# Performance work log

Measured on AMD Instinct MI355X. Metric: run time of the kernel, lower is better.

The kernel has to match this reference:

```python
import jax, jax.numpy as jnp
import numpy as np

N = 100_000      # nodes
E = 1_600_000    # graph edges
M = 10_000       # hyperedges
I = 800_000      # hypergraph incidences
F_IN = 128
HID = 128


def _lin(key, fan_in, fan_out):
    return (jax.random.normal(key, (fan_in, fan_out), jnp.float32) / np.sqrt(fan_in)).astype(jnp.float32)


def setup_inputs() -> dict:
    key = jax.random.key(0)
    ks = jax.random.split(key, 14)
    x = jax.random.normal(ks[0], (N, F_IN), jnp.float32)
    edge_index = jax.random.randint(ks[1], (2, E), 0, N, dtype=jnp.int32)
    edge_weights = jax.random.uniform(ks[2], (E,), jnp.float32)
    node_idx = jax.random.randint(ks[3], (I,), 0, N, dtype=jnp.int32)
    he_idx = jax.random.randint(ks[4], (I,), 0, M, dtype=jnp.int32)
    hyperedge_index = jnp.stack([node_idx, he_idx])
    hyperedge_distances = jax.random.uniform(ks[5], (M,), jnp.float32)
    return {
        "x": x,
        "edge_index": edge_index,
        "edge_weights": edge_weights,
        "hyperedge_index": hyperedge_index,
        "hyperedge_distances": hyperedge_distances,
        "W_g1": _lin(ks[6], F_IN, HID), "b_g1": jnp.zeros((HID,), jnp.float32),
        "W_g2": _lin(ks[7], HID, HID), "b_g2": jnp.zeros((HID,), jnp.float32),
        "W_h1": _lin(ks[8], F_IN, HID), "b_h1": jnp.zeros((HID,), jnp.float32),
        "W_h2": _lin(ks[9], HID, HID), "b_h2": jnp.zeros((HID,), jnp.float32),
        "W_fc": _lin(ks[10], 2 * HID, HID), "b_fc": jnp.zeros((HID,), jnp.float32),
        "W_out": _lin(ks[11], HID, 2), "b_out": jnp.zeros((2,), jnp.float32),
    }


def _gcn(h_in, W, b, row, col, ew):
    # PyG GCNConv: lin -> sym-normalized scatter-add (self-loops included in row/col/ew) -> +bias
    h = h_in @ W
    deg = jax.ops.segment_sum(ew, col, num_segments=N)
    dis = jnp.where(deg > 0, jax.lax.rsqrt(deg), 0.0)
    norm = dis[row] * ew * dis[col]
    out = jax.ops.segment_sum(norm[:, None] * h[row], col, num_segments=N)
    return out + b


def _hyper(h_in, W, b, node_idx, he_idx):
    # PyG HypergraphConv (use_attention=False, hyperedge_weight=1):
    # out = D^{-1} H B^{-1} H^T (X W) + b
    h = h_in @ W
    D = jax.ops.segment_sum(jnp.ones((node_idx.shape[0],), h.dtype), node_idx, num_segments=N)
    Dinv = jnp.where(D > 0, 1.0 / D, 0.0)
    Bc = jax.ops.segment_sum(jnp.ones((he_idx.shape[0],), h.dtype), he_idx, num_segments=M)
    Binv = jnp.where(Bc > 0, 1.0 / Bc, 0.0)
    edge_feat = Binv[:, None] * jax.ops.segment_sum(h[node_idx], he_idx, num_segments=M)
    out = Dinv[:, None] * jax.ops.segment_sum(edge_feat[he_idx], node_idx, num_segments=N)
    return out + b


def reference(x, edge_index, edge_weights, hyperedge_index, hyperedge_distances,
              W_g1, b_g1, W_g2, b_g2, W_h1, b_h1, W_h2, b_h2,
              W_fc, b_fc, W_out, b_out):
    # add self-loops (GCNConv default add_self_loops=True, fill=1)
    loops = jnp.arange(N, dtype=edge_index.dtype)
    row = jnp.concatenate([edge_index[0], loops])
    col = jnp.concatenate([edge_index[1], loops])
    ew = jnp.concatenate([edge_weights, jnp.ones((N,), edge_weights.dtype)])

    # GCN branch (dropout = identity in eval)
    x1 = jax.nn.relu(_gcn(x, W_g1, b_g1, row, col, ew))
    x1 = jax.nn.relu(_gcn(x1, W_g2, b_g2, row, col, ew))

    # vectorized form of the per-incidence python loop:
    # node_hyperedge_weights[v] = sum over incidences (v, e) of hyperedge_distances[e]
    node_idx, he_idx = hyperedge_index[0], hyperedge_index[1]
    nhw = jax.ops.segment_sum(hyperedge_distances[he_idx], node_idx, num_segments=N)
    x2 = x * nhw[:, None]

    x2 = jax.nn.relu(_hyper(x2, W_h1, b_h1, node_idx, he_idx))
    x2 = jax.nn.relu(_hyper(x2, W_h2, b_h2, node_idx, he_idx))

    h = jnp.concatenate([x1, x2], axis=1)
    h = jax.nn.relu(h @ W_fc + b_fc)
    return h @ W_out + b_out
```

## Files before the change

kernel.cpp:

```cpp
#include <hip/hip_runtime.h>
#include <hip/hip_fp16.h>


#define THREADS 256
#define CAP_E  64
#define CAP_IN 40
#define CAP_IH 144

#define BC_E 4608
#define BC_I 2432
#define BC_H 3072

#define P1_ITEMS 16
#define P1_BLOCK 4096

typedef _Float16 half8 __attribute__((ext_vector_type(8)));
typedef float floatx4 __attribute__((ext_vector_type(4)));

#define FIX_SCALE 16777216.0f

template <int MODE>
__device__ __forceinline__ void phase1_core(
    int blk, const int* __restrict__ keys, const int* __restrict__ vals,
    const float* __restrict__ wts,
    unsigned long long* __restrict__ buf64, unsigned int* __restrict__ buf32,
    int* __restrict__ bincnt, int nitems, int nbins, int bincap,
    unsigned int* hist, unsigned int* off, unsigned int* gb, unsigned int* wsum,
    unsigned long long* reord, unsigned short* rbin) {
  const int tid = threadIdx.x;
  const int base = blk * P1_BLOCK;
  for (int i = tid; i < 512; i += 256) hist[i] = 0;
  __syncthreads();
  unsigned long long pl[P1_ITEMS];
  int bn[P1_ITEMS], lr[P1_ITEMS];
#pragma unroll
  for (int j = 0; j < P1_ITEMS; ++j) {
    int idx = base + j * 256 + tid;
    bn[j] = -1;
    if (idx < nitems) {
      int k = keys[idx], v = vals[idx];
      if (MODE == 0) {
        bn[j] = k >> 8;
        pl[j] = ((unsigned long long)__float_as_uint(wts[idx]) << 32) |
                ((unsigned long long)((unsigned int)v << 8)) |
                (unsigned long long)(k & 255);
      } else if (MODE == 1) {
        bn[j] = k >> 8;
        pl[j] = (unsigned long long)(((unsigned int)v << 8) | (unsigned int)(k & 255));
      } else {
        bn[j] = k >> 5;
        pl[j] = (unsigned long long)(((unsigned int)v << 5) | (unsigned int)(k & 31));
      }
      lr[j] = (int)atomicAdd(&hist[bn[j]], 1u);
    }
  }
  __syncthreads();
  unsigned int v0 = hist[2 * tid], v1 = hist[2 * tid + 1];
  unsigned int tsum = v0 + v1;
  unsigned int incl = tsum;
  for (int o = 1; o < 64; o <<= 1) {
    unsigned int t = __shfl_up(incl, o, 64);
    if ((tid & 63) >= o) incl += t;
  }
  if ((tid & 63) == 63) wsum[tid >> 6] = incl;
  __syncthreads();
  unsigned int woff = 0;
  for (int w = 0; w < (tid >> 6); ++w) woff += wsum[w];
  unsigned int texcl = incl - tsum + woff;
  off[2 * tid] = texcl;
  off[2 * tid + 1] = texcl + v0;
  if (2 * tid < nbins && v0) gb[2 * tid] = (unsigned int)atomicAdd(&bincnt[2 * tid], (int)v0);
  if (2 * tid + 1 < nbins && v1) gb[2 * tid + 1] = (unsigned int)atomicAdd(&bincnt[2 * tid + 1], (int)v1);
  __syncthreads();
#pragma unroll
  for (int j = 0; j < P1_ITEMS; ++j) {
    if (bn[j] >= 0) {
      unsigned int pos = off[bn[j]] + (unsigned int)lr[j];
      reord[pos] = pl[j];
      rbin[pos] = (unsigned short)bn[j];
    }
  }
  __syncthreads();
  int total = nitems - base;
  if (total > P1_BLOCK) total = P1_BLOCK;
#pragma unroll
  for (int j = 0; j < P1_ITEMS; ++j) {
    int p = j * 256 + tid;
    if (p < total) {
      int b = rbin[p];
      unsigned int idx = gb[b] + (unsigned int)p - off[b];
      if (idx < (unsigned int)bincap) {
        if (MODE == 0) buf64[(size_t)b * bincap + idx] = reord[p];
        else buf32[(size_t)b * bincap + idx] = (unsigned int)reord[p];
      }
    }
  }
}

__global__ __launch_bounds__(256) void bin_phase1_all(
    const int* __restrict__ col, const int* __restrict__ row, const float* __restrict__ ew,
    const int* __restrict__ vidx, const int* __restrict__ heidx,
    unsigned long long* __restrict__ buf_e, unsigned int* __restrict__ buf_in,
    unsigned int* __restrict__ buf_ih,
    int* __restrict__ bincnt_e, int* __restrict__ bincnt_in, int* __restrict__ bincnt_ih,
    int E, int I, int GB_E, int GB_I, int NB_E, int NB_I, int NB_H) {
  __shared__ unsigned int hist[512];
  __shared__ unsigned int off[512];
  __shared__ unsigned int gb[512];
  __shared__ unsigned int wsum[4];
  __shared__ unsigned long long reord[P1_BLOCK];
  __shared__ unsigned short rbin[P1_BLOCK];
  int b = blockIdx.x;
  if (b < GB_E)
    phase1_core<0>(b, col, row, ew, buf_e, nullptr, bincnt_e, E, NB_E, BC_E,
                   hist, off, gb, wsum, reord, rbin);
  else if (b < GB_E + GB_I)
    phase1_core<1>(b - GB_E, vidx, heidx, nullptr, nullptr, buf_in, bincnt_in, I, NB_I, BC_I,
                   hist, off, gb, wsum, reord, rbin);
  else
    phase1_core<2>(b - GB_E - GB_I, heidx, vidx, nullptr, nullptr, buf_ih, bincnt_ih, I, NB_H, BC_H,
                   hist, off, gb, wsum, reord, rbin);
}

__global__ __launch_bounds__(256) void bin_phase2_all(
    const unsigned long long* __restrict__ buf_e, const unsigned int* __restrict__ buf_in,
    const unsigned int* __restrict__ buf_ih,
    const int* __restrict__ bincnt_e, const int* __restrict__ bincnt_in,
    const int* __restrict__ bincnt_ih, const float* __restrict__ hd,
    int2* __restrict__ epairs, int* __restrict__ he_by_node, int* __restrict__ v_by_he,
    int* __restrict__ ecnt, float* __restrict__ dis,
    int* __restrict__ ncnt, float* __restrict__ nhwf, float* __restrict__ Dinv,
    int* __restrict__ hecnt, float* __restrict__ Binv,
    int N, int M, int NB_E, int NB_I) {
  __shared__ unsigned int cnt[256];
  __shared__ unsigned int aux[256];
  const int tid = threadIdx.x;
  int b = blockIdx.x;
  if (b < NB_E) {
    cnt[tid] = 0; aux[tid] = 0;
    __syncthreads();
    int tot = bincnt_e[b]; if (tot > BC_E) tot = BC_E;
    const unsigned long long* seg = buf_e + (size_t)b * BC_E;
    for (int i = tid; i < tot; i += 256) {
      unsigned long long pl = seg[i];
      int c_lo = (int)(pl & 255u);
      int r = (int)((pl >> 8) & 0xFFFFFFu);
      float w = __uint_as_float((unsigned int)(pl >> 32));
      unsigned int s = atomicAdd(&cnt[c_lo], 1u);
      atomicAdd(&aux[c_lo], (unsigned int)(w * FIX_SCALE + 0.5f));
      if (s < CAP_E)
        epairs[((size_t)b * 256 + c_lo) * CAP_E + s] = make_int2(r, __float_as_int(w));
    }
    __syncthreads();
    int v = b * 256 + tid;
    if (v < N) {
      unsigned int c = cnt[tid];
      ecnt[v] = (c < CAP_E) ? (int)c : CAP_E;
      dis[v] = rsqrtf(1.0f + (float)aux[tid] * (1.0f / FIX_SCALE));
    }
  } else if (b < NB_E + NB_I) {
    b -= NB_E;
    cnt[tid] = 0; aux[tid] = 0;
    __syncthreads();
    int tot = bincnt_in[b]; if (tot > BC_I) tot = BC_I;
    const unsigned int* seg = buf_in + (size_t)b * BC_I;
    for (int i = tid; i < tot; i += 256) {
      unsigned int pl = seg[i];
      int v_lo = (int)(pl & 255u);
      int e = (int)(pl >> 8);
      unsigned int s = atomicAdd(&cnt[v_lo], 1u);
      atomicAdd(&aux[v_lo], (unsigned int)(hd[e] * FIX_SCALE + 0.5f));
      if (s < CAP_IN) he_by_node[((size_t)b * 256 + v_lo) * CAP_IN + s] = e;
    }
    __syncthreads();
    int v = b * 256 + tid;
    if (v < N) {
      unsigned int c = cnt[tid];
      ncnt[v] = (c < CAP_IN) ? (int)c : CAP_IN;
      nhwf[v] = (float)aux[tid] * (1.0f / FIX_SCALE);
      Dinv[v] = (c > 0) ? 1.0f / (float)c : 0.0f;
    }
  } else {
    b -= NB_E + NB_I;
    if (tid < 32) cnt[tid] = 0;
    __syncthreads();
    int tot = bincnt_ih[b]; if (tot > BC_H) tot = BC_H;
    const unsigned int* seg = buf_ih + (size_t)b * BC_H;
    for (int i = tid; i < tot; i += 256) {
      unsigned int pl = seg[i];
      int e_lo = (int)(pl & 31u);
      int v = (int)(pl >> 5);
      unsigned int s = atomicAdd(&cnt[e_lo], 1u);
      if (s < CAP_IH) v_by_he[((size_t)b * 32 + e_lo) * CAP_IH + s] = v;
    }
    __syncthreads();
    if (tid < 32) {
      int e = b * 32 + tid;
      if (e < M) {
        unsigned int c = cnt[tid];
        hecnt[e] = (c < CAP_IH) ? (int)c : CAP_IH;
        Binv[e] = (c > 0) ? 1.0f / (float)c : 0.0f;
      }
    }
  }
}

__global__ void wprep_all(const float* __restrict__ Wg1, const float* __restrict__ Wg2,
                          const float* __restrict__ Wh1, const float* __restrict__ Wh2,
                          const float* __restrict__ Wfc,
                          _Float16* __restrict__ Wtg1, _Float16* __restrict__ Wtg2,
                          _Float16* __restrict__ Wth1, _Float16* __restrict__ Wth2,
                          _Float16* __restrict__ Wtfc) {
  int idx = blockIdx.x * THREADS + threadIdx.x;
  if (idx < 65536) {
    int s = idx >> 14, local = idx & 16383;
    const float* W = (s == 0) ? Wg1 : (s == 1) ? Wg2 : (s == 2) ? Wh1 : Wh2;
    _Float16* Wt = (s == 0) ? Wtg1 : (s == 1) ? Wtg2 : (s == 2) ? Wth1 : Wth2;
    int n = local >> 7, kk = local & 127;
    int k = kk ^ ((n & 7) << 3);
    Wt[local] = (_Float16)W[k * 128 + n];
  } else if (idx < 98304) {
    int local = idx - 65536;
    int n = local >> 8, kk = local & 255;
    int k = kk ^ ((n & 7) << 3);
    Wtfc[local] = (_Float16)Wfc[k * 128 + n];
  }
}

__global__ __launch_bounds__(256) void mm_dual(
    const float* __restrict__ X, const _Float16* __restrict__ Wt1,
    const _Float16* __restrict__ Wt2, const float* __restrict__ dis,
    _Float16* __restrict__ C1, _Float16* __restrict__ C2, int nrows) {
  __shared__ _Float16 WtL[2][128 * 128];
  __shared__ _Float16 ebuf[4][16 * 136];
  const int tid = threadIdx.x;
  {
    const float4* s1 = (const float4*)Wt1;
    const float4* s2 = (const float4*)Wt2;
    float4* d1 = (float4*)WtL[0];
    float4* d2 = (float4*)WtL[1];
#pragma unroll
    for (int i = 0; i < 8; ++i) { d1[tid + 256 * i] = s1[tid + 256 * i]; d2[tid + 256 * i] = s2[tid + 256 * i]; }
  }
  __syncthreads();
  const int w = tid >> 6, l = tid & 63;
  const int m = l & 15, quad = l >> 4;
  const int rbase = blockIdx.x * 256 + w * 64;
  half8 a[4][4];
#pragma unroll
  for (int r = 0; r < 4; ++r) {
    int gr = rbase + r * 16 + m;
#pragma unroll
    for (int s = 0; s < 4; ++s) {
      int ks = s * 32 + quad * 8;
      if (gr < nrows) {
        float4 f0 = *(const float4*)(X + (size_t)gr * 128 + ks);
        float4 f1 = *(const float4*)(X + (size_t)gr * 128 + ks + 4);
        half8 h;
        h[0] = (_Float16)f0.x; h[1] = (_Float16)f0.y; h[2] = (_Float16)f0.z; h[3] = (_Float16)f0.w;
        h[4] = (_Float16)f1.x; h[5] = (_Float16)f1.y; h[6] = (_Float16)f1.z; h[7] = (_Float16)f1.w;
        a[r][s] = h;
      } else {
#pragma unroll
        for (int j = 0; j < 8; ++j) a[r][s][j] = (_Float16)0.0f;
      }
    }
  }
  _Float16* eb = ebuf[w];
#pragma unroll
  for (int pass = 0; pass < 2; ++pass) {
    floatx4 acc[4][8];
#pragma unroll
    for (int r = 0; r < 4; ++r)
#pragma unroll
      for (int c = 0; c < 8; ++c)
#pragma unroll
        for (int j = 0; j < 4; ++j) acc[r][c][j] = 0.0f;
#pragma unroll
    for (int s = 0; s < 4; ++s) {
      const int ks = s * 32 + quad * 8;
#pragma unroll
      for (int c = 0; c < 8; ++c) {
        int n = c * 16 + m;
        half8 b = *(const half8*)&WtL[pass][n * 128 + (ks ^ ((n & 7) << 3))];
#pragma unroll
        for (int r = 0; r < 4; ++r)
          acc[r][c] = __builtin_amdgcn_mfma_f32_16x16x32_f16(a[r][s], b, acc[r][c], 0, 0, 0);
      }
    }
    _Float16* Cout = pass ? C2 : C1;
#pragma unroll
    for (int r = 0; r < 4; ++r) {
      float dv[4];
#pragma unroll
      for (int j = 0; j < 4; ++j) {
        int grow = rbase + r * 16 + quad * 4 + j;
        dv[j] = (pass == 0 && grow < nrows) ? dis[grow] : 1.0f;
      }
#pragma unroll
      for (int c = 0; c < 8; ++c)
#pragma unroll
        for (int j = 0; j < 4; ++j)
          eb[(quad * 4 + j) * 136 + c * 16 + m] = (_Float16)(acc[r][c][j] * dv[j]);
#pragma unroll
      for (int t = 0; t < 4; ++t) {
        int chunk = t * 64 + l;
        int rr = chunk >> 4;
        int off = (chunk & 15) * 8;
        int gr = rbase + r * 16 + rr;
        half8 v = *(const half8*)&eb[rr * 136 + off];
        if (gr < nrows) *(half8*)(Cout + (size_t)gr * 128 + off) = v;
      }
    }
  }
}

template <int SCALE>
__global__ __launch_bounds__(256) void mm_mfma(
    const _Float16* __restrict__ A, const _Float16* __restrict__ Wt,
    const float* __restrict__ scale, _Float16* __restrict__ Cout, int nrows) {
  __shared__ _Float16 WtL[128 * 128];
  __shared__ _Float16 ebuf[4][16 * 136];
  const int tid = threadIdx.x;
  {
    const float4* src = (const float4*)Wt;
    float4* dst = (float4*)WtL;
#pragma unroll
    for (int i = 0; i < 8; ++i) dst[tid + 256 * i] = src[tid + 256 * i];
  }
  __syncthreads();
  const int w = tid >> 6, l = tid & 63;
  const int m = l & 15, quad = l >> 4;
  const int rbase = blockIdx.x * 256 + w * 64;
  floatx4 acc[4][8];
#pragma unroll
  for (int r = 0; r < 4; ++r)
#pragma unroll
    for (int c = 0; c < 8; ++c)
#pragma unroll
      for (int j = 0; j < 4; ++j) acc[r][c][j] = 0.0f;
#pragma unroll
  for (int s = 0; s < 4; ++s) {
    const int ks = s * 32 + quad * 8;
    half8 a[4];
#pragma unroll
    for (int r = 0; r < 4; ++r) {
      int gr = rbase + r * 16 + m;
      if (gr < nrows) {
        a[r] = *(const half8*)(A + (size_t)gr * 128 + ks);
      } else {
#pragma unroll
        for (int j = 0; j < 8; ++j) a[r][j] = (_Float16)0.0f;
      }
    }
#pragma unroll
    for (int c = 0; c < 8; ++c) {
      int n = c * 16 + m;
      half8 b = *(const half8*)&WtL[n * 128 + (ks ^ ((n & 7) << 3))];
#pragma unroll
      for (int r = 0; r < 4; ++r)
        acc[r][c] = __builtin_amdgcn_mfma_f32_16x16x32_f16(a[r], b, acc[r][c], 0, 0, 0);
    }
  }
  _Float16* eb = ebuf[w];
#pragma unroll
  for (int r = 0; r < 4; ++r) {
    float dv[4];
#pragma unroll
    for (int j = 0; j < 4; ++j) {
      int grow = rbase + r * 16 + quad * 4 + j;
      dv[j] = (SCALE && grow < nrows) ? scale[grow] : 1.0f;
    }
#pragma unroll
    for (int c = 0; c < 8; ++c)
#pragma unroll
      for (int j = 0; j < 4; ++j)
        eb[(quad * 4 + j) * 136 + c * 16 + m] = (_Float16)(SCALE ? acc[r][c][j] * dv[j] : acc[r][c][j]);
#pragma unroll
    for (int t = 0; t < 4; ++t) {
      int chunk = t * 64 + l;
      int rr = chunk >> 4;
      int off = (chunk & 15) * 8;
      int gr = rbase + r * 16 + rr;
      half8 v = *(const half8*)&eb[rr * 136 + off];
      if (gr < nrows) *(half8*)(Cout + (size_t)gr * 128 + off) = v;
    }
  }
}

__global__ __launch_bounds__(256) void fc_head(
    const _Float16* __restrict__ A1, const _Float16* __restrict__ A2,
    const _Float16* __restrict__ Wt, const float* __restrict__ bfc,
    const float* __restrict__ Wout, const float* __restrict__ bout,
    float* __restrict__ out, int nrows) {
  __shared__ _Float16 WtL[128 * 256];
  __shared__ float WoutL[256];
  const int tid = threadIdx.x;
  {
    const float4* src = (const float4*)Wt;
    float4* dst = (float4*)WtL;
#pragma unroll
    for (int i = 0; i < 16; ++i) dst[tid + 256 * i] = src[tid + 256 * i];
    WoutL[tid] = Wout[tid];
  }
  __syncthreads();
  const int w = tid >> 6, l = tid & 63;
  const int m = l & 15, quad = l >> 4;
  const int rbase = blockIdx.x * 256 + w * 64;
  floatx4 acc[4][8];
#pragma unroll
  for (int r = 0; r < 4; ++r)
#pragma unroll
    for (int c = 0; c < 8; ++c)
#pragma unroll
      for (int j = 0; j < 4; ++j) acc[r][c][j] = 0.0f;
#pragma unroll
  for (int s = 0; s < 8; ++s) {
    const _Float16* Asrc = (s >= 4) ? A2 : A1;
    const int kl = (s >= 4) ? (s - 4) * 32 + quad * 8 : s * 32 + quad * 8;
    const int ks = s * 32 + quad * 8;
    half8 a[4];
#pragma unroll
    for (int r = 0; r < 4; ++r) {
      int gr = rbase + r * 16 + m;
      if (gr < nrows) {
        a[r] = *(const half8*)(Asrc + (size_t)gr * 128 + kl);
      } else {
#pragma unroll
        for (int j = 0; j < 8; ++j) a[r][j] = (_Float16)0.0f;
      }
    }
#pragma unroll
    for (int c = 0; c < 8; ++c) {
      int n = c * 16 + m;
      half8 b = *(const half8*)&WtL[n * 256 + (ks ^ ((n & 7) << 3))];
#pragma unroll
      for (int r = 0; r < 4; ++r)
        acc[r][c] = __builtin_amdgcn_mfma_f32_16x16x32_f16(a[r], b, acc[r][c], 0, 0, 0);
    }
  }
  float b0 = bout[0], b1 = bout[1];
  float bias_c[8];
#pragma unroll
  for (int c = 0; c < 8; ++c) bias_c[c] = bfc[c * 16 + m];
#pragma unroll
  for (int r = 0; r < 4; ++r) {
#pragma unroll
    for (int j = 0; j < 4; ++j) {
      float s0 = 0.f, s1 = 0.f;
#pragma unroll
      for (int c = 0; c < 8; ++c) {
        float h = fmaxf(acc[r][c][j] + bias_c[c], 0.f);
        int k = c * 16 + m;
        s0 = fmaf(h, WoutL[k * 2 + 0], s0);
        s1 = fmaf(h, WoutL[k * 2 + 1], s1);
      }
#pragma unroll
      for (int off = 1; off < 16; off <<= 1) {
        s0 += __shfl_xor(s0, off, 64);
        s1 += __shfl_xor(s1, off, 64);
      }
      if (m == 0) {
        int gr = rbase + r * 16 + quad * 4 + j;
        if (gr < nrows) {
          float2 o = make_float2(s0 + b0, s1 + b1);
          *(float2*)(out + (size_t)gr * 2) = o;
        }
      }
    }
  }
}

__global__ __launch_bounds__(256) void gcn_gather16(
    const _Float16* __restrict__ h, const int* __restrict__ ecnt,
    const int2* __restrict__ epairs, const float* __restrict__ dis,
    const float* __restrict__ bias, _Float16* __restrict__ out, int N) {
  int g = threadIdx.x >> 4, l = threadIdx.x & 15;
  int c = blockIdx.x * 16 + g;
  if (c >= N) return;
  const float4* h4 = (const float4*)h;
  float4 self = h4[(size_t)c * 16 + l];
  const _Float16* sp = (const _Float16*)&self;
  float acc[8];
#pragma unroll
  for (int j = 0; j < 8; ++j) acc[j] = (float)sp[j];
  int cnt = ecnt[c];
  const int2* seg = epairs + (size_t)c * CAP_E;
  int p = 0;
  for (; p + 2 <= cnt; p += 2) {
    int2 pr0 = seg[p];
    int2 pr1 = seg[p + 1];
    float4 hv0 = h4[(size_t)pr0.x * 16 + l];
    float4 hv1 = h4[(size_t)pr1.x * 16 + l];
    float w0 = __int_as_float(pr0.y), w1 = __int_as_float(pr1.y);
    const _Float16* hp0 = (const _Float16*)&hv0;
    const _Float16* hp1 = (const _Float16*)&hv1;
#pragma unroll
    for (int j = 0; j < 8; ++j) acc[j] = fmaf(w0, (float)hp0[j], acc[j]);
#pragma unroll
    for (int j = 0; j < 8; ++j) acc[j] = fmaf(w1, (float)hp1[j], acc[j]);
  }
  if (p < cnt) {
    int2 pr = seg[p];
    float wgt = __int_as_float(pr.y);
    float4 hv = h4[(size_t)pr.x * 16 + l];
    const _Float16* hp = (const _Float16*)&hv;
#pragma unroll
    for (int j = 0; j < 8; ++j) acc[j] = fmaf(wgt, (float)hp[j], acc[j]);
  }
  float dc = dis[c];
  float4 b0 = ((const float4*)bias)[2 * l];
  float4 b1 = ((const float4*)bias)[2 * l + 1];
  float bb[8] = {b0.x, b0.y, b0.z, b0.w, b1.x, b1.y, b1.z, b1.w};
  half8 ov;
#pragma unroll
  for (int j = 0; j < 8; ++j) ov[j] = (_Float16)fmaxf(fmaf(acc[j], dc, bb[j]), 0.f);
  *(half8*)(out + (size_t)c * 128 + l * 8) = ov;
}

template <int SCALED>
__global__ __launch_bounds__(256) void hyper_ef16(
    const _Float16* __restrict__ h, const int* __restrict__ hecnt,
    const int* __restrict__ v_by_he, const float* __restrict__ Binv,
    const float* __restrict__ nhwf, _Float16* __restrict__ ef, int M) {
  int g = threadIdx.x >> 4, l = threadIdx.x & 15;
  int e = blockIdx.x * 16 + g;
  if (e >= M) return;
  const float4* h4 = (const float4*)h;
  float acc[8];
#pragma unroll
  for (int j = 0; j < 8; ++j) acc[j] = 0.f;
  int cnt = hecnt[e];
  const int* seg = v_by_he + (size_t)e * CAP_IH;
  int p = 0;
  for (; p + 4 <= cnt; p += 4) {
    int v0 = seg[p], v1 = seg[p + 1], v2 = seg[p + 2], v3 = seg[p + 3];
    float4 a0 = h4[(size_t)v0 * 16 + l];
    float4 a1 = h4[(size_t)v1 * 16 + l];
    float4 a2 = h4[(size_t)v2 * 16 + l];
    float4 a3 = h4[(size_t)v3 * 16 + l];
    float s0 = 1.f, s1 = 1.f, s2 = 1.f, s3 = 1.f;
    if (SCALED) { s0 = nhwf[v0]; s1 = nhwf[v1]; s2 = nhwf[v2]; s3 = nhwf[v3]; }
    const _Float16* p0 = (const _Float16*)&a0;
    const _Float16* p1 = (const _Float16*)&a1;
    const _Float16* p2 = (const _Float16*)&a2;
    const _Float16* p3 = (const _Float16*)&a3;
    if (SCALED) {
#pragma unroll
      for (int j = 0; j < 8; ++j)
        acc[j] += s0 * (float)p0[j] + s1 * (float)p1[j] + s2 * (float)p2[j] + s3 * (float)p3[j];
    } else {
#pragma unroll
      for (int j = 0; j < 8; ++j)
        acc[j] += ((float)p0[j] + (float)p1[j]) + ((float)p2[j] + (float)p3[j]);
    }
  }
  for (; p < cnt; ++p) {
    int v = seg[p];
    float4 hv = h4[(size_t)v * 16 + l];
    const _Float16* hp = (const _Float16*)&hv;
    if (SCALED) {
      float s = nhwf[v];
#pragma unroll
      for (int j = 0; j < 8; ++j) acc[j] = fmaf(s, (float)hp[j], acc[j]);
    } else {
#pragma unroll
      for (int j = 0; j < 8; ++j) acc[j] += (float)hp[j];
    }
  }
  float bi = Binv[e];
  half8 ov;
#pragma unroll
  for (int j = 0; j < 8; ++j) ov[j] = (_Float16)(acc[j] * bi);
  *(half8*)(ef + (size_t)e * 128 + l * 8) = ov;
}

__global__ __launch_bounds__(256) void hyper_out16(
    const _Float16* __restrict__ ef, const int* __restrict__ ncnt,
    const int* __restrict__ he_by_node, const float* __restrict__ Dinv,
    const float* __restrict__ bias, _Float16* __restrict__ out, int N) {
  int g = threadIdx.x >> 4, l = threadIdx.x & 15;
  int v = blockIdx.x * 16 + g;
  if (v >= N) return;
  const float4* ef4 = (const float4*)ef;
  float acc[8];
#pragma unroll
  for (int j = 0; j < 8; ++j) acc[j] = 0.f;
  int cnt = ncnt[v];
  const int* seg = he_by_node + (size_t)v * CAP_IN;
  int p = 0;
  for (; p + 2 <= cnt; p += 2) {
    int e0 = seg[p], e1 = seg[p + 1];
    float4 a0 = ef4[(size_t)e0 * 16 + l];
    float4 a1 = ef4[(size_t)e1 * 16 + l];
    const _Float16* p0 = (const _Float16*)&a0;
    const _Float16* p1 = (const _Float16*)&a1;
#pragma unroll
    for (int j = 0; j < 8; ++j) acc[j] += (float)p0[j] + (float)p1[j];
  }
  if (p < cnt) {
    int e = seg[p];
    float4 hv = ef4[(size_t)e * 16 + l];
    const _Float16* hp = (const _Float16*)&hv;
#pragma unroll
    for (int j = 0; j < 8; ++j) acc[j] += (float)hp[j];
  }
  float di = Dinv[v];
  float4 b0 = ((const float4*)bias)[2 * l];
  float4 b1 = ((const float4*)bias)[2 * l + 1];
  float bb[8] = {b0.x, b0.y, b0.z, b0.w, b1.x, b1.y, b1.z, b1.w};
  half8 ov;
#pragma unroll
  for (int j = 0; j < 8; ++j) ov[j] = (_Float16)fmaxf(fmaf(acc[j], di, bb[j]), 0.f);
  *(half8*)(out + (size_t)v * 128 + l * 8) = ov;
}

extern "C" void kernel_launch(void* const* d_in, const int* in_sizes, int n_in,
                              void* d_out, int out_size, void* d_ws, size_t ws_size,
                              hipStream_t stream) {
  const float* x    = (const float*)d_in[0];
  const int*   eidx = (const int*)d_in[1];
  const float* ew   = (const float*)d_in[2];
  const int*   hidx = (const int*)d_in[3];
  const float* hd   = (const float*)d_in[4];
  const float* Wg1  = (const float*)d_in[5];
  const float* bg1  = (const float*)d_in[6];
  const float* Wg2  = (const float*)d_in[7];
  const float* bg2  = (const float*)d_in[8];
  const float* Wh1  = (const float*)d_in[9];
  const float* bh1  = (const float*)d_in[10];
  const float* Wh2  = (const float*)d_in[11];
  const float* bh2  = (const float*)d_in[12];
  const float* Wfc  = (const float*)d_in[13];
  const float* bfc  = (const float*)d_in[14];
  const float* Wout = (const float*)d_in[15];
  const float* bout = (const float*)d_in[16];

  const int N = in_sizes[0] / 128;
  const int E = in_sizes[2];
  const int I = in_sizes[3] / 2;
  const int M = in_sizes[4];
  const int* row   = eidx;
  const int* col   = eidx + E;
  const int* vidx  = hidx;
  const int* heidx = hidx + I;

  const int NB_E = (N + 255) >> 8;
  const int NB_I = (N + 255) >> 8;
  const int NB_H = (M + 31) >> 5;
  const int GB_E = (E + P1_BLOCK - 1) / P1_BLOCK;
  const int GB_I = (I + P1_BLOCK - 1) / P1_BLOCK;

  char* p = (char*)d_ws;
  auto alloc = [&](size_t bytes) -> void* {
    void* r = (void*)p;
    p += (bytes + 255) & ~(size_t)255;
    return r;
  };
  float* dis   = (float*)alloc((size_t)N * 4);
  float* nhwf  = (float*)alloc((size_t)N * 4);
  float* Dinv  = (float*)alloc((size_t)N * 4);
  float* Binv  = (float*)alloc((size_t)M * 4);
  int* ecnt    = (int*)alloc((size_t)N * 4);
  int* ncnt    = (int*)alloc((size_t)N * 4);
  int* hecnt   = (int*)alloc((size_t)M * 4);
  int* bincnt_e  = (int*)alloc((size_t)(NB_E + NB_I + NB_H) * 4);
  int* bincnt_in = bincnt_e + NB_E;
  int* bincnt_ih = bincnt_in + NB_I;
  int2* epairs = (int2*)alloc((size_t)N * CAP_E * 8);
  int* he_by_node = (int*)alloc((size_t)N * CAP_IN * 4);
  int* v_by_he    = (int*)alloc((size_t)M * CAP_IH * 4);
  _Float16* Bg   = (_Float16*)alloc((size_t)N * 128 * 2);
  _Float16* Bh   = (_Float16*)alloc((size_t)N * 128 * 2);
  _Float16* Btmp = (_Float16*)alloc((size_t)N * 128 * 2);
  _Float16* Bt1  = (_Float16*)alloc((size_t)N * 128 * 2);
  _Float16* Bt2  = (_Float16*)alloc((size_t)N * 128 * 2);
  _Float16* ef16 = (_Float16*)alloc((size_t)M * 128 * 2);
  _Float16* Wtg1 = (_Float16*)alloc(128 * 128 * 2);
  _Float16* Wtg2 = (_Float16*)alloc(128 * 128 * 2);
  _Float16* Wth1 = (_Float16*)alloc(128 * 128 * 2);
  _Float16* Wth2 = (_Float16*)alloc(128 * 128 * 2);
  _Float16* Wtfc = (_Float16*)alloc(128 * 256 * 2);

  unsigned long long* buf_e  = (unsigned long long*)Bt1;
  unsigned int*       buf_in = (unsigned int*)Bt2;
  unsigned int*       buf_ih = (unsigned int*)((char*)Bt2 + (4 << 20));

  wprep_all<<<384, THREADS, 0, stream>>>(Wg1, Wg2, Wh1, Wh2, Wfc, Wtg1, Wtg2, Wth1, Wth2, Wtfc);

  hipMemsetAsync(bincnt_e, 0, (size_t)(NB_E + NB_I + NB_H) * 4, stream);
  bin_phase1_all<<<GB_E + 2 * GB_I, THREADS, 0, stream>>>(
      col, row, ew, vidx, heidx, buf_e, buf_in, buf_ih,
      bincnt_e, bincnt_in, bincnt_ih, E, I, GB_E, GB_I, NB_E, NB_I, NB_H);
  bin_phase2_all<<<NB_E + NB_I + NB_H, THREADS, 0, stream>>>(
      buf_e, buf_in, buf_ih, bincnt_e, bincnt_in, bincnt_ih, hd,
      epairs, he_by_node, v_by_he, ecnt, dis, ncnt, nhwf, Dinv, hecnt, Binv,
      N, M, NB_E, NB_I);

  const int GMM = (N + 255) / 256;
  const int GN16 = (N + 15) / 16;
  const int GM16 = (M + 15) / 16;

  mm_dual<<<GMM, THREADS, 0, stream>>>(x, Wtg1, Wth1, dis, Bg, Bh, N);

  gcn_gather16<<<GN16, THREADS, 0, stream>>>(Bg, ecnt, epairs, dis, bg1, Bt1, N);
  mm_mfma<1><<<GMM, THREADS, 0, stream>>>(Bt1, Wtg2, dis, Btmp, N);
  gcn_gather16<<<GN16, THREADS, 0, stream>>>(Btmp, ecnt, epairs, dis, bg2, Bt1, N);

  hyper_ef16<1><<<GM16, THREADS, 0, stream>>>(Bh, hecnt, v_by_he, Binv, nhwf, ef16, M);
  hyper_out16<<<GN16, THREADS, 0, stream>>>(ef16, ncnt, he_by_node, Dinv, bh1, Bt2, N);
  mm_mfma<0><<<GMM, THREADS, 0, stream>>>(Bt2, Wth2, nullptr, Btmp, N);
  hyper_ef16<0><<<GM16, THREADS, 0, stream>>>(Btmp, hecnt, v_by_he, Binv, nullptr, ef16, M);
  hyper_out16<<<GN16, THREADS, 0, stream>>>(ef16, ncnt, he_by_node, Dinv, bh2, Bt2, N);

  fc_head<<<GMM, THREADS, 0, stream>>>(Bt1, Bt2, Wtfc, bfc, Wout, bout, (float*)d_out, N);
}
```

Measured before the change: 525.4 us.

## Merge independent GCN and hypergraph stages into shared launches and trim shared memory

Independent GCN and hypergraph kernels are now launched together through block-index dispatch: gather with hyperedge-reduce, and the two second-layer matmuls. This fills the GPU with more concurrent work and removes launches. The bincount memset is folded into the weight-prep kernel. mm_dual and fc_head now stream one 128x128 weight slice through shared memory at a time, which lowers LDS use so more blocks fit per CU. The dis pre-scaling moves from the first matmul epilogue into the first gather, which adds per-neighbour dis loads there.

```diff
diff --git a/kernel.cpp b/kernel.cpp
--- a/kernel.cpp
+++ b/kernel.cpp
@@ -13,6 +13,8 @@
 
 #define P1_ITEMS 16
 #define P1_BLOCK 4096
+
+#define SMEM_MM 50176
 
 typedef _Float16 half8 __attribute__((ext_vector_type(8)));
 typedef float floatx4 __attribute__((ext_vector_type(4)));
@@ -205,12 +207,16 @@
   }
 }
 
-__global__ void wprep_all(const float* __restrict__ Wg1, const float* __restrict__ Wg2,
-                          const float* __restrict__ Wh1, const float* __restrict__ Wh2,
-                          const float* __restrict__ Wfc,
-                          _Float16* __restrict__ Wtg1, _Float16* __restrict__ Wtg2,
-                          _Float16* __restrict__ Wth1, _Float16* __restrict__ Wth2,
-                          _Float16* __restrict__ Wtfc) {
+__global__ void prep_k(const float* __restrict__ Wg1, const float* __restrict__ Wg2,
+                       const float* __restrict__ Wh1, const float* __restrict__ Wh2,
+                       const float* __restrict__ Wfc,
+                       _Float16* __restrict__ Wtg1, _Float16* __restrict__ Wtg2,
+                       _Float16* __restrict__ Wth1, _Float16* __restrict__ Wth2,
+                       _Float16* __restrict__ Wtfc, int* __restrict__ bincnt, int nbins) {
+  if (blockIdx.x == gridDim.x - 1) {
+    for (int i = threadIdx.x; i < nbins; i += 256) bincnt[i] = 0;
+    return;
+  }
   int idx = blockIdx.x * THREADS + threadIdx.x;
   if (idx < 65536) {
     int s = idx >> 14, local = idx & 16383;
@@ -227,22 +233,87 @@
   }
 }
 
+__device__ __forceinline__ void mm_core(
+    int blk, const _Float16* __restrict__ A, const _Float16* __restrict__ Wt,
+    const float* __restrict__ scale, _Float16* __restrict__ Cout, int nrows,
+    unsigned char* smem) {
+  _Float16* WtL = (_Float16*)smem;
+  _Float16* ebuf = (_Float16*)(smem + 32768);
+  const int tid = threadIdx.x;
+  {
+    const float4* src = (const float4*)Wt;
+    float4* dst = (float4*)WtL;
+#pragma unroll
+    for (int i = 0; i < 8; ++i) dst[tid + 256 * i] = src[tid + 256 * i];
+  }
+  __syncthreads();
+  const int w = tid >> 6, l = tid & 63;
+  const int m = l & 15, quad = l >> 4;
+  const int rbase = blk * 256 + w * 64;
+  floatx4 acc[4][8];
+#pragma unroll
+  for (int r = 0; r < 4; ++r)
+#pragma unroll
+    for (int c = 0; c < 8; ++c)
+#pragma unroll
+      for (int j = 0; j < 4; ++j) acc[r][c][j] = 0.0f;
+#pragma unroll
+  for (int s = 0; s < 4; ++s) {
+    const int ks = s * 32 + quad * 8;
+    half8 a[4];
+#pragma unroll
+    for (int r = 0; r < 4; ++r) {
+      int gr = rbase + r * 16 + m;
+      if (gr < nrows) {
+        a[r] = *(const half8*)(A + (size_t)gr * 128 + ks);
+      } else {
+#pragma unroll
+        for (int j = 0; j < 8; ++j) a[r][j] = (_Float16)0.0f;
+      }
+    }
+#pragma unroll
+    for (int c = 0; c < 8; ++c) {
+      int n = c * 16 + m;
+      half8 b = *(const half8*)&WtL[n * 128 + (ks ^ ((n & 7) << 3))];
+#pragma unroll
+      for (int r = 0; r < 4; ++r)
+        acc[r][c] = __builtin_amdgcn_mfma_f32_16x16x32_f16(a[r], b, acc[r][c], 0, 0, 0);
+    }
+  }
+  _Float16* eb = ebuf + w * (16 * 136);
+#pragma unroll
+  for (int r = 0; r < 4; ++r) {
+    float dv[4];
+#pragma unroll
+    for (int j = 0; j < 4; ++j) {
+      int grow = rbase + r * 16 + quad * 4 + j;
+      dv[j] = (scale && grow < nrows) ? scale[grow] : 1.0f;
+    }
+#pragma unroll
+    for (int c = 0; c < 8; ++c)
+#pragma unroll
+      for (int j = 0; j < 4; ++j)
+        eb[(quad * 4 + j) * 136 + c * 16 + m] = (_Float16)(acc[r][c][j] * dv[j]);
+#pragma unroll
+    for (int t = 0; t < 4; ++t) {
+      int chunk = t * 64 + l;
+      int rr = chunk >> 4;
+      int off = (chunk & 15) * 8;
+      int gr = rbase + r * 16 + rr;
+      half8 v = *(const half8*)&eb[rr * 136 + off];
+      if (gr < nrows) *(half8*)(Cout + (size_t)gr * 128 + off) = v;
+    }
+  }
+}
+
 __global__ __launch_bounds__(256) void mm_dual(
     const float* __restrict__ X, const _Float16* __restrict__ Wt1,
-    const _Float16* __restrict__ Wt2, const float* __restrict__ dis,
-    _Float16* __restrict__ C1, _Float16* __restrict__ C2, int nrows) {
-  __shared__ _Float16 WtL[2][128 * 128];
-  __shared__ _Float16 ebuf[4][16 * 136];
+    const _Float16* __restrict__ Wt2, _Float16* __restrict__ C1,
+    _Float16* __restrict__ C2, int nrows) {
+  __shared__ __align__(16) unsigned char smem[SMEM_MM];
+  _Float16* WtL = (_Float16*)smem;
+  _Float16* ebuf = (_Float16*)(smem + 32768);
   const int tid = threadIdx.x;
-  {
-    const float4* s1 = (const float4*)Wt1;
-    const float4* s2 = (const float4*)Wt2;
-    float4* d1 = (float4*)WtL[0];
-    float4* d2 = (float4*)WtL[1];
-#pragma unroll
-    for (int i = 0; i < 8; ++i) { d1[tid + 256 * i] = s1[tid + 256 * i]; d2[tid + 256 * i] = s2[tid + 256 * i]; }
-  }
-  __syncthreads();
   const int w = tid >> 6, l = tid & 63;
   const int m = l & 15, quad = l >> 4;
   const int rbase = blockIdx.x * 256 + w * 64;
@@ -266,9 +337,15 @@
       }
     }
   }
-  _Float16* eb = ebuf[w];
-#pragma unroll
+  _Float16* eb = ebuf + w * (16 * 136);
   for (int pass = 0; pass < 2; ++pass) {
+    {
+      const float4* src = (const float4*)(pass ? Wt2 : Wt1);
+      float4* dst = (float4*)WtL;
+#pragma unroll
+      for (int i = 0; i < 8; ++i) dst[tid + 256 * i] = src[tid + 256 * i];
+    }
+    __syncthreads();
     floatx4 acc[4][8];
 #pragma unroll
     for (int r = 0; r < 4; ++r)
@@ -282,7 +359,7 @@
 #pragma unroll
       for (int c = 0; c < 8; ++c) {
         int n = c * 16 + m;
-        half8 b = *(const half8*)&WtL[pass][n * 128 + (ks ^ ((n & 7) << 3))];
+        half8 b = *(const half8*)&WtL[n * 128 + (ks ^ ((n & 7) << 3))];
 #pragma unroll
         for (int r = 0; r < 4; ++r)
           acc[r][c] = __builtin_amdgcn_mfma_f32_16x16x32_f16(a[r][s], b, acc[r][c], 0, 0, 0);
@@ -291,17 +368,11 @@
     _Float16* Cout = pass ? C2 : C1;
 #pragma unroll
     for (int r = 0; r < 4; ++r) {
-      float dv[4];
-#pragma unroll
-      for (int j = 0; j < 4; ++j) {
-        int grow = rbase + r * 16 + quad * 4 + j;
-        dv[j] = (pass == 0 && grow < nrows) ? dis[grow] : 1.0f;
-      }
 #pragma unroll
       for (int c = 0; c < 8; ++c)
 #pragma unroll
         for (int j = 0; j < 4; ++j)
-          eb[(quad * 4 + j) * 136 + c * 16 + m] = (_Float16)(acc[r][c][j] * dv[j]);
+          eb[(quad * 4 + j) * 136 + c * 16 + m] = (_Float16)acc[r][c][j];
 #pragma unroll
       for (int t = 0; t < 4; ++t) {
         int chunk = t * 64 + l;
@@ -312,178 +383,36 @@
         if (gr < nrows) *(half8*)(Cout + (size_t)gr * 128 + off) = v;
       }
     }
-  }
-}
-
-template <int SCALE>
-__global__ __launch_bounds__(256) void mm_mfma(
-    const _Float16* __restrict__ A, const _Float16* __restrict__ Wt,
-    const float* __restrict__ scale, _Float16* __restrict__ Cout, int nrows) {
-  __shared__ _Float16 WtL[128 * 128];
-  __shared__ _Float16 ebuf[4][16 * 136];
-  const int tid = threadIdx.x;
-  {
-    const float4* src = (const float4*)Wt;
-    float4* dst = (float4*)WtL;
-#pragma unroll
-    for (int i = 0; i < 8; ++i) dst[tid + 256 * i] = src[tid + 256 * i];
-  }
-  __syncthreads();
-  const int w = tid >> 6, l = tid & 63;
-  const int m = l & 15, quad = l >> 4;
-  const int rbase = blockIdx.x * 256 + w * 64;
-  floatx4 acc[4][8];
-#pragma unroll
-  for (int r = 0; r < 4; ++r)
-#pragma unroll
-    for (int c = 0; c < 8; ++c)
-#pragma unroll
-      for (int j = 0; j < 4; ++j) acc[r][c][j] = 0.0f;
-#pragma unroll
-  for (int s = 0; s < 4; ++s) {
-    const int ks = s * 32 + quad * 8;
-    half8 a[4];
-#pragma unroll
-    for (int r = 0; r < 4; ++r) {
-      int gr = rbase + r * 16 + m;
-      if (gr < nrows) {
-        a[r] = *(const half8*)(A + (size_t)gr * 128 + ks);
-      } else {
-#pragma unroll
-        for (int j = 0; j < 8; ++j) a[r][j] = (_Float16)0.0f;
-      }
-    }
-#pragma unroll
-    for (int c = 0; c < 8; ++c) {
-      int n = c * 16 + m;
-      half8 b = *(const half8*)&WtL[n * 128 + (ks ^ ((n & 7) << 3))];
-#pragma unroll
-      for (int r = 0; r < 4; ++r)
-        acc[r][c] = __builtin_amdgcn_mfma_f32_16x16x32_f16(a[r], b, acc[r][c], 0, 0, 0);
-    }
-  }
-  _Float16* eb = ebuf[w];
-#pragma unroll
-  for (int r = 0; r < 4; ++r) {
-    float dv[4];
-#pragma unroll
-    for (int j = 0; j < 4; ++j) {
-      int grow = rbase + r * 16 + quad * 4 + j;
-      dv[j] = (SCALE && grow < nrows) ? scale[grow] : 1.0f;
-    }
-#pragma unroll
-    for (int c = 0; c < 8; ++c)
-#pragma unroll
-      for (int j = 0; j < 4; ++j)
-        eb[(quad * 4 + j) * 136 + c * 16 + m] = (_Float16)(SCALE ? acc[r][c][j] * dv[j] : acc[r][c][j]);
-#pragma unroll
-    for (int t = 0; t < 4; ++t) {
-      int chunk = t * 64 + l;
-      int rr = chunk >> 4;
-      int off = (chunk & 15) * 8;
-      int gr = rbase + r * 16 + rr;
-      half8 v = *(const half8*)&eb[rr * 136 + off];
-      if (gr < nrows) *(half8*)(Cout + (size_t)gr * 128 + off) = v;
-    }
-  }
-}
-
-__global__ __launch_bounds__(256) void fc_head(
-    const _Float16* __restrict__ A1, const _Float16* __restrict__ A2,
-    const _Float16* __restrict__ Wt, const float* __restrict__ bfc,
-    const float* __restrict__ Wout, const float* __restrict__ bout,
-    float* __restrict__ out, int nrows) {
-  __shared__ _Float16 WtL[128 * 256];
-  __shared__ float WoutL[256];
-  const int tid = threadIdx.x;
-  {
-    const float4* src = (const float4*)Wt;
-    float4* dst = (float4*)WtL;
-#pragma unroll
-    for (int i = 0; i < 16; ++i) dst[tid + 256 * i] = src[tid + 256 * i];
-    WoutL[tid] = Wout[tid];
-  }
-  __syncthreads();
-  const int w = tid >> 6, l = tid & 63;
-  const int m = l & 15, quad = l >> 4;
-  const int rbase = blockIdx.x * 256 + w * 64;
-  floatx4 acc[4][8];
-#pragma unroll
-  for (int r = 0; r < 4; ++r)
-#pragma unroll
-    for (int c = 0; c < 8; ++c)
-#pragma unroll
-      for (int j = 0; j < 4; ++j) acc[r][c][j] = 0.0f;
-#pragma unroll
-  for (int s = 0; s < 8; ++s) {
-    const _Float16* Asrc = (s >= 4) ? A2 : A1;
-    const int kl = (s >= 4) ? (s - 4) * 32 + quad * 8 : s * 32 + quad * 8;
-    const int ks = s * 32 + quad * 8;
-    half8 a[4];
-#pragma unroll
-    for (int r = 0; r < 4; ++r) {
-      int gr = rbase + r * 16 + m;
-      if (gr < nrows) {
-        a[r] = *(const half8*)(Asrc + (size_t)gr * 128 + kl);
-      } else {
-#pragma unroll
-        for (int j = 0; j < 8; ++j) a[r][j] = (_Float16)0.0f;
-      }
-    }
-#pragma unroll
-    for (int c = 0; c < 8; ++c) {
-      int n = c * 16 + m;
-      half8 b = *(const half8*)&WtL[n * 256 + (ks ^ ((n & 7) << 3))];
-#pragma unroll
-      for (int r = 0; r < 4; ++r)
-        acc[r][c] = __builtin_amdgcn_mfma_f32_16x16x32_f16(a[r], b, acc[r][c], 0, 0, 0);
-    }
-  }
-  float b0 = bout[0], b1 = bout[1];
-  float bias_c[8];
-#pragma unroll
-  for (int c = 0; c < 8; ++c) bias_c[c] = bfc[c * 16 + m];
-#pragma unroll
-  for (int r = 0; r < 4; ++r) {
-#pragma unroll
-    for (int j = 0; j < 4; ++j) {
-      float s0 = 0.f, s1 = 0.f;
-#pragma unroll
-      for (int c = 0; c < 8; ++c) {
-        float h = fmaxf(acc[r][c][j] + bias_c[c], 0.f);
-        int k = c * 16 + m;
-        s0 = fmaf(h, WoutL[k * 2 + 0], s0);
-        s1 = fmaf(h, WoutL[k * 2 + 1], s1);
-      }
-#pragma unroll
-      for (int off = 1; off < 16; off <<= 1) {
-        s0 += __shfl_xor(s0, off, 64);
-        s1 += __shfl_xor(s1, off, 64);
-      }
-      if (m == 0) {
-        int gr = rbase + r * 16 + quad * 4 + j;
-        if (gr < nrows) {
-          float2 o = make_float2(s0 + b0, s1 + b1);
-          *(float2*)(out + (size_t)gr * 2) = o;
-        }
-      }
-    }
-  }
-}
-
-__global__ __launch_bounds__(256) void gcn_gather16(
-    const _Float16* __restrict__ h, const int* __restrict__ ecnt,
+    __syncthreads();
+  }
+}
+
+__global__ __launch_bounds__(256) void mm_pair(
+    const _Float16* __restrict__ A1, const _Float16* __restrict__ Wt1,
+    const float* __restrict__ scale1, _Float16* __restrict__ C1,
+    const _Float16* __restrict__ A2, const _Float16* __restrict__ Wt2,
+    _Float16* __restrict__ C2, int nrows, int GMM) {
+  __shared__ __align__(16) unsigned char smem[SMEM_MM];
+  int b = blockIdx.x;
+  if (b < GMM) mm_core(b, A1, Wt1, scale1, C1, nrows, smem);
+  else         mm_core(b - GMM, A2, Wt2, nullptr, C2, nrows, smem);
+}
+
+template <int PRESCALED>
+__device__ __forceinline__ void gcn_core(
+    int blk, const _Float16* __restrict__ h, const int* __restrict__ ecnt,
     const int2* __restrict__ epairs, const float* __restrict__ dis,
     const float* __restrict__ bias, _Float16* __restrict__ out, int N) {
   int g = threadIdx.x >> 4, l = threadIdx.x & 15;
-  int c = blockIdx.x * 16 + g;
+  int c = blk * 16 + g;
   if (c >= N) return;
   const float4* h4 = (const float4*)h;
+  float dc = dis[c];
   float4 self = h4[(size_t)c * 16 + l];
   const _Float16* sp = (const _Float16*)&self;
   float acc[8];
 #pragma unroll
-  for (int j = 0; j < 8; ++j) acc[j] = (float)sp[j];
+  for (int j = 0; j < 8; ++j) acc[j] = PRESCALED ? (float)sp[j] : dc * (float)sp[j];
   int cnt = ecnt[c];
   const int2* seg = epairs + (size_t)c * CAP_E;
   int p = 0;
@@ -493,6 +422,7 @@
     float4 hv0 = h4[(size_t)pr0.x * 16 + l];
     float4 hv1 = h4[(size_t)pr1.x * 16 + l];
     float w0 = __int_as_float(pr0.y), w1 = __int_as_float(pr1.y);
+    if (!PRESCALED) { w0 *= dis[pr0.x]; w1 *= dis[pr1.x]; }
     const _Float16* hp0 = (const _Float16*)&hv0;
     const _Float16* hp1 = (const _Float16*)&hv1;
 #pragma unroll
@@ -503,12 +433,12 @@
   if (p < cnt) {
     int2 pr = seg[p];
     float wgt = __int_as_float(pr.y);
+    if (!PRESCALED) wgt *= dis[pr.x];
     float4 hv = h4[(size_t)pr.x * 16 + l];
     const _Float16* hp = (const _Float16*)&hv;
 #pragma unroll
     for (int j = 0; j < 8; ++j) acc[j] = fmaf(wgt, (float)hp[j], acc[j]);
   }
-  float dc = dis[c];
   float4 b0 = ((const float4*)bias)[2 * l];
   float4 b1 = ((const float4*)bias)[2 * l + 1];
   float bb[8] = {b0.x, b0.y, b0.z, b0.w, b1.x, b1.y, b1.z, b1.w};
@@ -519,12 +449,12 @@
 }
 
 template <int SCALED>
-__global__ __launch_bounds__(256) void hyper_ef16(
-    const _Float16* __restrict__ h, const int* __restrict__ hecnt,
+__device__ __forceinline__ void hyperef_core(
+    int blk, const _Float16* __restrict__ h, const int* __restrict__ hecnt,
     const int* __restrict__ v_by_he, const float* __restrict__ Binv,
     const float* __restrict__ nhwf, _Float16* __restrict__ ef, int M) {
   int g = threadIdx.x >> 4, l = threadIdx.x & 15;
-  int e = blockIdx.x * 16 + g;
+  int e = blk * 16 + g;
   if (e >= M) return;
   const float4* h4 = (const float4*)h;
   float acc[8];
@@ -575,6 +505,31 @@
   *(half8*)(ef + (size_t)e * 128 + l * 8) = ov;
 }
 
+__global__ __launch_bounds__(256) void g_he_1(
+    const _Float16* __restrict__ Bg, const int* __restrict__ ecnt,
+    const int2* __restrict__ epairs, const float* __restrict__ dis,
+    const float* __restrict__ bg1, _Float16* __restrict__ Bt1,
+    const _Float16* __restrict__ Bh, const int* __restrict__ hecnt,
+    const int* __restrict__ v_by_he, const float* __restrict__ Binv,
+    const float* __restrict__ nhwf, _Float16* __restrict__ ef,
+    int N, int M, int GN16) {
+  int b = blockIdx.x;
+  if (b < GN16) gcn_core<0>(b, Bg, ecnt, epairs, dis, bg1, Bt1, N);
+  else hyperef_core<1>(b - GN16, Bh, hecnt, v_by_he, Binv, nhwf, ef, M);
+}
+
+__global__ __launch_bounds__(256) void g_he_2(
+    const _Float16* __restrict__ Btmp1, const int* __restrict__ ecnt,
+    const int2* __restrict__ epairs, const float* __restrict__ dis,
+    const float* __restrict__ bg2, _Float16* __restrict__ Bt1,
+    const _Float16* __restrict__ Btmp2, const int* __restrict__ hecnt,
+    const int* __restrict__ v_by_he, const float* __restrict__ Binv,
+    _Float16* __restrict__ ef, int N, int M, int GN16) {
+  int b = blockIdx.x;
+  if (b < GN16) gcn_core<1>(b, Btmp1, ecnt, epairs, dis, bg2, Bt1, N);
+  else hyperef_core<0>(b - GN16, Btmp2, hecnt, v_by_he, Binv, nullptr, ef, M);
+}
+
 __global__ __launch_bounds__(256) void hyper_out16(
     const _Float16* __restrict__ ef, const int* __restrict__ ncnt,
     const int* __restrict__ he_by_node, const float* __restrict__ Dinv,
@@ -613,6 +568,94 @@
 #pragma unroll
   for (int j = 0; j < 8; ++j) ov[j] = (_Float16)fmaxf(fmaf(acc[j], di, bb[j]), 0.f);
   *(half8*)(out + (size_t)v * 128 + l * 8) = ov;
+}
+
+__global__ __launch_bounds__(256) void fc_head(
+    const _Float16* __restrict__ A1, const _Float16* __restrict__ A2,
+    const _Float16* __restrict__ Wt, const float* __restrict__ bfc,
+    const float* __restrict__ Wout, const float* __restrict__ bout,
+    float* __restrict__ out, int nrows) {
+  __shared__ _Float16 WtL[128 * 128];
+  __shared__ float WoutL[256];
+  const int tid = threadIdx.x;
+  WoutL[tid] = Wout[tid];
+  const int w = tid >> 6, l = tid & 63;
+  const int m = l & 15, quad = l >> 4;
+  const int rbase = blockIdx.x * 256 + w * 64;
+  floatx4 acc[4][8];
+#pragma unroll
+  for (int r = 0; r < 4; ++r)
+#pragma unroll
+    for (int c = 0; c < 8; ++c)
+#pragma unroll
+      for (int j = 0; j < 4; ++j) acc[r][c][j] = 0.0f;
+  for (int half = 0; half < 2; ++half) {
+    {
+      const float4* src = (const float4*)Wt;
+      float4* dst = (float4*)WtL;
+#pragma unroll
+      for (int i = 0; i < 8; ++i) {
+        int idx = tid + 256 * i;
+        dst[idx] = src[(idx >> 4) * 32 + half * 16 + (idx & 15)];
+      }
+    }
+    __syncthreads();
+    const _Float16* Asrc = half ? A2 : A1;
+#pragma unroll
+    for (int ss = 0; ss < 4; ++ss) {
+      const int kl = ss * 32 + quad * 8;
+      half8 a[4];
+#pragma unroll
+      for (int r = 0; r < 4; ++r) {
+        int gr = rbase + r * 16 + m;
+        if (gr < nrows) {
+          a[r] = *(const half8*)(Asrc + (size_t)gr * 128 + kl);
+        } else {
+#pragma unroll
+          for (int j = 0; j < 8; ++j) a[r][j] = (_Float16)0.0f;
+        }
+      }
+#pragma unroll
+      for (int c = 0; c < 8; ++c) {
+        int n = c * 16 + m;
+        half8 b = *(const half8*)&WtL[n * 128 + (kl ^ ((n & 7) << 3))];
+#pragma unroll
+        for (int r = 0; r < 4; ++r)
+          acc[r][c] = __builtin_amdgcn_mfma_f32_16x16x32_f16(a[r], b, acc[r][c], 0, 0, 0);
+      }
+    }
+    __syncthreads();
+  }
+  float b0 = bout[0], b1 = bout[1];
+  float bias_c[8];
+#pragma unroll
+  for (int c = 0; c < 8; ++c) bias_c[c] = bfc[c * 16 + m];
+#pragma unroll
+  for (int r = 0; r < 4; ++r) {
+#pragma unroll
+    for (int j = 0; j < 4; ++j) {
+      float s0 = 0.f, s1 = 0.f;
+#pragma unroll
+      for (int c = 0; c < 8; ++c) {
+        float h = fmaxf(acc[r][c][j] + bias_c[c], 0.f);
+        int k = c * 16 + m;
+        s0 = fmaf(h, WoutL[k * 2 + 0], s0);
+        s1 = fmaf(h, WoutL[k * 2 + 1], s1);
+      }
+#pragma unroll
+      for (int off = 1; off < 16; off <<= 1) {
+        s0 += __shfl_xor(s0, off, 64);
+        s1 += __shfl_xor(s1, off, 64);
+      }
+      if (m == 0) {
+        int gr = rbase + r * 16 + quad * 4 + j;
+        if (gr < nrows) {
+          float2 o = make_float2(s0 + b0, s1 + b1);
+          *(float2*)(out + (size_t)gr * 2) = o;
+        }
+      }
+    }
+  }
 }
 
 extern "C" void kernel_launch(void* const* d_in, const int* in_sizes, int n_in,
@@ -672,7 +715,6 @@
   int* v_by_he    = (int*)alloc((size_t)M * CAP_IH * 4);
   _Float16* Bg   = (_Float16*)alloc((size_t)N * 128 * 2);
   _Float16* Bh   = (_Float16*)alloc((size_t)N * 128 * 2);
-  _Float16* Btmp = (_Float16*)alloc((size_t)N * 128 * 2);
   _Float16* Bt1  = (_Float16*)alloc((size_t)N * 128 * 2);
   _Float16* Bt2  = (_Float16*)alloc((size_t)N * 128 * 2);
   _Float16* ef16 = (_Float16*)alloc((size_t)M * 128 * 2);
@@ -686,32 +728,29 @@
   unsigned int*       buf_in = (unsigned int*)Bt2;
   unsigned int*       buf_ih = (unsigned int*)((char*)Bt2 + (4 << 20));
 
-  wprep_all<<<384, THREADS, 0, stream>>>(Wg1, Wg2, Wh1, Wh2, Wfc, Wtg1, Wtg2, Wth1, Wth2, Wtfc);
-
-  hipMemsetAsync(bincnt_e, 0, (size_t)(NB_E + NB_I + NB_H) * 4, stream);
+  const int GMM  = (N + 255) / 256;
+  const int GN16 = (N + 15) / 16;
+  const int GM16 = (M + 15) / 16;
+  const int NBINS = NB_E + NB_I + NB_H;
+
+  prep_k<<<385, THREADS, 0, stream>>>(Wg1, Wg2, Wh1, Wh2, Wfc,
+                                      Wtg1, Wtg2, Wth1, Wth2, Wtfc, bincnt_e, NBINS);
   bin_phase1_all<<<GB_E + 2 * GB_I, THREADS, 0, stream>>>(
       col, row, ew, vidx, heidx, buf_e, buf_in, buf_ih,
       bincnt_e, bincnt_in, bincnt_ih, E, I, GB_E, GB_I, NB_E, NB_I, NB_H);
-  bin_phase2_all<<<NB_E + NB_I + NB_H, THREADS, 0, stream>>>(
+  bin_phase2_all<<<NBINS, THREADS, 0, stream>>>(
       buf_e, buf_in, buf_ih, bincnt_e, bincnt_in, bincnt_ih, hd,
       epairs, he_by_node, v_by_he, ecnt, dis, ncnt, nhwf, Dinv, hecnt, Binv,
       N, M, NB_E, NB_I);
-
-  const int GMM = (N + 255) / 256;
-  const int GN16 = (N + 15) / 16;
-  const int GM16 = (M + 15) / 16;
-
-  mm_dual<<<GMM, THREADS, 0, stream>>>(x, Wtg1, Wth1, dis, Bg, Bh, N);
-
-  gcn_gather16<<<GN16, THREADS, 0, stream>>>(Bg, ecnt, epairs, dis, bg1, Bt1, N);
-  mm_mfma<1><<<GMM, THREADS, 0, stream>>>(Bt1, Wtg2, dis, Btmp, N);
-  gcn_gather16<<<GN16, THREADS, 0, stream>>>(Btmp, ecnt, epairs, dis, bg2, Bt1, N);
-
-  hyper_ef16<1><<<GM16, THREADS, 0, stream>>>(Bh, hecnt, v_by_he, Binv, nhwf, ef16, M);
+  mm_dual<<<GMM, THREADS, 0, stream>>>(x, Wtg1, Wth1, Bg, Bh, N);
+  g_he_1<<<GN16 + GM16, THREADS, 0, stream>>>(
+      Bg, ecnt, epairs, dis, bg1, Bt1,
+      Bh, hecnt, v_by_he, Binv, nhwf, ef16, N, M, GN16);
   hyper_out16<<<GN16, THREADS, 0, stream>>>(ef16, ncnt, he_by_node, Dinv, bh1, Bt2, N);
-  mm_mfma<0><<<GMM, THREADS, 0, stream>>>(Bt2, Wth2, nullptr, Btmp, N);
-  hyper_ef16<0><<<GM16, THREADS, 0, stream>>>(Btmp, hecnt, v_by_he, Binv, nullptr, ef16, M);
+  mm_pair<<<2 * GMM, THREADS, 0, stream>>>(Bt1, Wtg2, dis, Bg, Bt2, Wth2, Bh, N, GMM);
+  g_he_2<<<GN16 + GM16, THREADS, 0, stream>>>(
+      Bg, ecnt, epairs, dis, bg2, Bt1,
+      Bh, hecnt, v_by_he, Binv, ef16, N, M, GN16);
   hyper_out16<<<GN16, THREADS, 0, stream>>>(ef16, ncnt, he_by_node, Dinv, bh2, Bt2, N);
-
   fc_head<<<GMM, THREADS, 0, stream>>>(Bt1, Bt2, Wtfc, bfc, Wout, bout, (float*)d_out, N);
 }
```

New measurement: 523.5 us. About the same (-0.4%).
